# Kernel optimization log

Hardware: AMD Instinct MI355X
Metric: run time of the kernel (lower is better)

Reference implementation:

```python
import jax, jax.numpy as jnp
import numpy as np

BS, SEQ, IN_DIM, EMB = 64, 1024, 512, 1024
HID = EMB // 2  # MLP hidden = embed_dim//2 = 512
RATIO = 0.3
K = max(1, int((SEQ - 2) * RATIO))  # 306
MASK_VALUE = -10000.0
BN_EPS = 1e-5


def setup_inputs() -> dict:
    key = jax.random.key(0)
    ks = jax.random.split(key, 12)
    features = jax.random.normal(ks[0], (BS, SEQ, IN_DIM), dtype=jnp.float32)
    atten = jax.random.normal(ks[1], (BS, SEQ, SEQ), dtype=jnp.float32)
    # variable-length token ids, pad_id = 0
    lengths = jax.random.randint(ks[2], (BS,), K + 14, SEQ + 1)
    tokens = jax.random.randint(ks[3], (BS, SEQ), 1, 30000)
    text = jnp.where(jnp.arange(SEQ)[None, :] < lengths[:, None], tokens, 0).astype(jnp.int64)
    s = 0.02
    lin_w = jax.random.normal(ks[4], (IN_DIM, EMB), dtype=jnp.float32) * s
    lin_b = jnp.zeros((EMB,), dtype=jnp.float32)
    w1 = jax.random.normal(ks[5], (IN_DIM, HID), dtype=jnp.float32) * s
    b1 = jnp.zeros((HID,), dtype=jnp.float32)
    g1 = jnp.ones((HID,), dtype=jnp.float32)
    be1 = jnp.zeros((HID,), dtype=jnp.float32)
    w2 = jax.random.normal(ks[6], (HID, EMB), dtype=jnp.float32) * s
    b2 = jnp.zeros((EMB,), dtype=jnp.float32)
    return {"features": features, "atten": atten, "text": text,
            "lin_w": lin_w, "lin_b": lin_b, "w1": w1, "b1": b1,
            "g1": g1, "be1": be1, "w2": w2, "b2": b2}


def _forward(features, atten, text, lin_w, lin_b, w1, b1, g1, be1, w2, b2):
    bs, seq_len, _ = atten.shape
    atten = jnp.nan_to_num(atten, nan=0.0, posinf=0.0, neginf=0.0)
    mask = (text != 0).astype(jnp.float32)                       # (bs, seq)
    token_lens = jnp.maximum(jnp.sum(text != 0, axis=1), 1)       # (bs,)
    eos_pos = jnp.clip(token_lens - 1, 0, seq_len - 1)            # (bs,)
    # mask column 0 and column eos_pos (per batch) across all rows
    col = jnp.arange(seq_len)[None, :]
    col_mask = (col == 0) | (col == eos_pos[:, None])             # (bs, seq)
    atten = jnp.where(col_mask[:, None, :], MASK_VALUE, atten)
    # masked_fill where token is pad (columns)
    atten = jnp.where(mask[:, None, :] == 0, MASK_VALUE, atten)
    atten = jax.nn.softmax(atten, axis=1)                         # softmax over rows (dim=1)
    # select the eos row per batch, weight by mask
    atten_sel = jnp.take_along_axis(atten, eos_pos[:, None, None], axis=1)[:, 0, :] * mask
    _, topk_idx = jax.lax.top_k(atten_sel, K)                     # (bs, K)
    feats_k = jnp.take_along_axis(features, topk_idx[:, :, None], axis=1)  # (bs, K, D)
    norm = jnp.maximum(jnp.linalg.norm(feats_k, axis=-1, keepdims=True), 1e-6)
    feats_k = feats_k / norm
    cap_emb = feats_k @ lin_w + lin_b                             # (bs, K, EMB)
    # MLP: Linear -> BatchNorm1d(train-mode batch stats) -> ReLU -> Linear
    xf = feats_k.reshape(bs * K, -1)
    h = xf @ w1 + b1                                              # (bs*K, HID)
    mu = jnp.mean(h, axis=0)
    var = jnp.mean((h - mu) ** 2, axis=0)                         # biased var
    h = (h - mu) / jnp.sqrt(var + BN_EPS) * g1 + be1
    h = jax.nn.relu(h)
    feats_mlp = (h @ w2 + b2).reshape(bs, K, -1)
    fused = cap_emb + feats_mlp                                   # (bs, K, EMB)
    # variable-length top-1 pooling: max over first pool_lens[b] tokens
    pool_lens = jnp.clip(token_lens - 2, 1, K)
    valid = jnp.arange(K)[None, :] < pool_lens[:, None]           # (bs, K)
    out = jnp.max(jnp.where(valid[:, :, None], fused, -jnp.inf), axis=1)
    return out.astype(jnp.float32)


def reference(features, atten, text, lin_w, lin_b, w1, b1, g1, be1, w2, b2):
    return _forward(features, atten, text, lin_w, lin_b, w1, b1, g1, be1, w2, b2)
```

## Files before the change

### kernel.cpp

```cpp
#include <hip/hip_runtime.h>
#include <hip/hip_cooperative_groups.h>
#include <cstdint>
#include <cstddef>
#include <cmath>

namespace cg = cooperative_groups;

#define BS 64
#define SEQ 1024
#define IN_DIM 512
#define EMB 1024
#define HID 512
#define KSEL 306
#define MROWS (BS * KSEL)

typedef __bf16 bf16_t;
typedef bf16_t bf16x8 __attribute__((ext_vector_type(8)));
typedef bf16_t bf16x4 __attribute__((ext_vector_type(4)));
typedef float f32x4 __attribute__((ext_vector_type(4)));

__device__ __forceinline__ void async16(const void* g, void* l) {
  __builtin_amdgcn_global_load_lds(
      (const __attribute__((address_space(1))) unsigned int*)g,
      (__attribute__((address_space(3))) unsigned int*)l, 16, 0, 0);
}

__device__ __forceinline__ void atomicMaxF(float* a, float v) {
  if (v >= 0.f)
    atomicMax((int*)a, __float_as_int(v));
  else
    atomicMin((unsigned int*)a, __float_as_uint(v));
}

__global__ void k_meta(const int* __restrict__ text, int* __restrict__ eos,
                       float* __restrict__ out) {
  int b = blockIdx.x;
  __shared__ int cnt;
  if (threadIdx.x == 0) cnt = 0;
  __syncthreads();
  int local = 0;
  for (int i = threadIdx.x; i < SEQ; i += blockDim.x)
    local += (text[b * SEQ + i] != 0) ? 1 : 0;
  atomicAdd(&cnt, local);
  for (int c = threadIdx.x; c < EMB; c += blockDim.x)
    out[(b << 10) + c] = -INFINITY;
  __syncthreads();
  if (threadIdx.x == 0) {
    int L = cnt > 1 ? cnt : 1;
    int e = L - 1;
    if (e > SEQ - 1) e = SEQ - 1;
    eos[b] = e;
  }
}

__global__ void k_colsum(const float* __restrict__ atten, float* __restrict__ part) {
  int b = blockIdx.x;
  int r0 = blockIdx.y << 6;
  int c = threadIdx.x << 2;
  const float* base = atten + ((size_t)b << 20) + ((size_t)r0 << 10) + c;
  float4 s = {0.f, 0.f, 0.f, 0.f};
#pragma unroll 4
  for (int r = 0; r < 64; ++r) {
    float4 x = *(const float4*)(base + ((size_t)r << 10));
    s.x += __expf((isfinite(x.x) ? x.x : 0.f) - 12.f);
    s.y += __expf((isfinite(x.y) ? x.y : 0.f) - 12.f);
    s.z += __expf((isfinite(x.z) ? x.z : 0.f) - 12.f);
    s.w += __expf((isfinite(x.w) ? x.w : 0.f) - 12.f);
  }
  *(float4*)&part[((((size_t)blockIdx.y << 6) | b) << 10) | c] = s;
}

__global__ void k_topk(const float* __restrict__ atten, const int* __restrict__ text,
                       const int* __restrict__ eos, const float* __restrict__ part,
                       int* __restrict__ selidx) {
  int b = blockIdx.x;
  __shared__ float vals[SEQ];
  int e = eos[b];
  for (int c = threadIdx.x; c < SEQ; c += 256) {
    float cs = 0.f;
#pragma unroll
    for (int p = 0; p < 16; ++p) cs += part[(((p << 6) | b) << 10) | c];
    float v = atten[((size_t)b << 20) + ((size_t)e << 10) + c];
    if (!isfinite(v)) v = 0.f;
    int tok = text[(b << 10) | c];
    float res;
    if (tok == 0) res = 0.f;
    else if (c == 0 || c == e) res = 1.f / 1024.f;
    else res = __expf(v - 12.f) / cs;
    vals[c] = res;
  }
  __syncthreads();
  int i = (blockIdx.y << 8) | threadIdx.x;
  float vc = vals[i];
  int rank = 0;
  for (int j = 0; j < SEQ; ++j) {
    float vj = vals[j];
    rank += (vj > vc || (vj == vc && j < i)) ? 1 : 0;
  }
  if (rank < KSEL) selidx[b * KSEL + rank] = i;
}

__global__ void k_gather(const float* __restrict__ features, const int* __restrict__ sel,
                         bf16_t* __restrict__ xcat) {
  int row = blockIdx.x;
  int b = row / KSEL;
  int k = row - b * KSEL;
  int idx = sel[b * KSEL + k];
  const float4* src = (const float4*)(features + (((size_t)b << 10) + idx) * IN_DIM);
  float4 v = src[threadIdx.x];
  float ss = v.x * v.x + v.y * v.y + v.z * v.z + v.w * v.w;
#pragma unroll
  for (int off = 32; off > 0; off >>= 1) ss += __shfl_down(ss, off, 64);
  __shared__ float wsum[2];
  int lane = threadIdx.x & 63, wid = threadIdx.x >> 6;
  if (lane == 0) wsum[wid] = ss;
  __syncthreads();
  float total = wsum[0] + wsum[1];
  float scale = 1.f / fmaxf(sqrtf(total), 1e-6f);
  bf16x4 o;
  o[0] = (bf16_t)(v.x * scale);
  o[1] = (bf16_t)(v.y * scale);
  o[2] = (bf16_t)(v.z * scale);
  o[3] = (bf16_t)(v.w * scale);
  *(bf16x4*)(xcat + (size_t)row * EMB + (threadIdx.x << 2)) = o;
}

__global__ void k_transpose_all(const float* __restrict__ w1, const float* __restrict__ lin_w,
                                const float* __restrict__ w2, bf16_t* __restrict__ w1t,
                                bf16_t* __restrict__ wcatt) {
  __shared__ float tile[32][33];
  int by = blockIdx.y;
  const float* src; int srcld; bf16_t* dst; int dstld; int n0;
  if (by < 16)      { src = w1;    srcld = HID; dst = w1t;         dstld = IN_DIM; n0 = by << 5; }
  else if (by < 48) { src = lin_w; srcld = EMB; dst = wcatt;       dstld = EMB;    n0 = (by - 16) << 5; }
  else              { src = w2;    srcld = EMB; dst = wcatt + 512; dstld = EMB;    n0 = (by - 48) << 5; }
  int k0 = blockIdx.x << 5;
  int tx = threadIdx.x, ty = threadIdx.y;
#pragma unroll
  for (int i = 0; i < 4; i++)
    tile[ty + 8 * i][tx] = src[(size_t)(k0 + ty + 8 * i) * srcld + n0 + tx];
  __syncthreads();
#pragma unroll
  for (int i = 0; i < 4; i++)
    dst[(size_t)(n0 + ty + 8 * i) * dstld + k0 + tx] = (bf16_t)tile[tx][ty + 8 * i];
}

__global__ __launch_bounds__(512, 1) void k_gemm1_coop(
    const bf16_t* A,
    const bf16_t* __restrict__ Bt,
    const float* __restrict__ b1, const float* __restrict__ g1,
    const float* __restrict__ be1, float* stats,
    bf16_t* xcat_out) {
  __shared__ __align__(16) bf16_t As[128 * 32];
  __shared__ __align__(16) bf16_t Bs[512 * 32];
  int tid = threadIdx.x;
  int m0 = blockIdx.x << 7;
  int wave = tid >> 6, lane = tid & 63;
  int wm = (wave >> 2) << 6;
  int wn = (wave & 3) << 7;
  int lrow = lane & 15, quad = lane >> 4;

  f32x4 acc[4][8];
#pragma unroll
  for (int i = 0; i < 4; i++)
#pragma unroll
    for (int j = 0; j < 8; j++) acc[i][j] = (f32x4){0.f, 0.f, 0.f, 0.f};

  int arow = tid >> 2, ak = (tid & 3) << 3;
  const bf16_t* Ap = A + (size_t)(m0 + arow) * EMB + ak;
  int brow0 = tid >> 2, bk = (tid & 3) << 3;
  const bf16_t* Bp0 = Bt + (size_t)(brow0 + 0) * IN_DIM + bk;
  const bf16_t* Bp1 = Bt + (size_t)(brow0 + 128) * IN_DIM + bk;
  const bf16_t* Bp2 = Bt + (size_t)(brow0 + 256) * IN_DIM + bk;
  const bf16_t* Bp3 = Bt + (size_t)(brow0 + 384) * IN_DIM + bk;

  for (int k0 = 0; k0 < IN_DIM; k0 += 32) {
    async16(Ap + k0, &As[tid << 3]);
    async16(Bp0 + k0, &Bs[(tid + 0) << 3]);
    async16(Bp1 + k0, &Bs[(tid + 512) << 3]);
    async16(Bp2 + k0, &Bs[(tid + 1024) << 3]);
    async16(Bp3 + k0, &Bs[(tid + 1536) << 3]);
    __syncthreads();

    bf16x8 af[4], bfr[8];
#pragma unroll
    for (int i = 0; i < 4; i++)
      af[i] = *(const bf16x8*)&As[((wm + (i << 4) + lrow) << 5) + (quad << 3)];
#pragma unroll
    for (int j = 0; j < 8; j++)
      bfr[j] = *(const bf16x8*)&Bs[((wn + (j << 4) + lrow) << 5) + (quad << 3)];
#pragma unroll
    for (int i = 0; i < 4; i++)
#pragma unroll
      for (int j = 0; j < 8; j++)
        acc[i][j] = __builtin_amdgcn_mfma_f32_16x16x32_bf16(af[i], bfr[j], acc[i][j], 0, 0, 0);
    __syncthreads();
  }

#pragma unroll
  for (int j = 0; j < 8; j++) {
    int n = wn + (j << 4) + lrow;
    float bv = b1[n];
    float s = 0.f, qq = 0.f;
#pragma unroll
    for (int i = 0; i < 4; i++) {
#pragma unroll
      for (int rr = 0; rr < 4; rr++) {
        float v = acc[i][j][rr] + bv;
        acc[i][j][rr] = v;
        s += v;
        qq += v * v;
      }
    }
    s += __shfl_xor(s, 16, 64);
    s += __shfl_xor(s, 32, 64);
    qq += __shfl_xor(qq, 16, 64);
    qq += __shfl_xor(qq, 32, 64);
    if (quad == 0) {
      atomicAdd(&stats[n], s);
      atomicAdd(&stats[HID + n], qq);
    }
  }

  cg::this_grid().sync();

  const float inv = 1.f / (float)MROWS;
#pragma unroll
  for (int j = 0; j < 8; j++) {
    int n = wn + (j << 4) + lrow;
    float mu = stats[n] * inv;
    float var = fmaxf(stats[HID + n] * inv - mu * mu, 0.f);
    float sc = g1[n] * rsqrtf(var + 1e-5f);
    float sh = fmaf(-mu, sc, be1[n]);
#pragma unroll
    for (int i = 0; i < 4; i++) {
      int mbase = m0 + wm + (i << 4) + (quad << 2);
#pragma unroll
      for (int rr = 0; rr < 4; rr++) {
        float a = fmaxf(fmaf(acc[i][j][rr], sc, sh), 0.f);
        xcat_out[(size_t)(mbase + rr) * EMB + 512 + n] = (bf16_t)a;
      }
    }
  }
}

__global__ __launch_bounds__(256, 2) void k_gemm2(
    const bf16_t* __restrict__ A, const bf16_t* __restrict__ Bt,
    const float* __restrict__ lin_b, const float* __restrict__ b2,
    float* __restrict__ outmax) {
  __shared__ __align__(16) bf16_t As[128 * 32];
  __shared__ __align__(16) bf16_t Bs[128 * 32];
  int tid = threadIdx.x;

  int MT = gridDim.x, NT = gridDim.y;
  int nwg = MT * NT;
  int flat = blockIdx.y * MT + blockIdx.x;
  int q = nwg >> 3, r = nwg & 7;
  int xcd = flat & 7, ii = flat >> 3;
  int lin = (xcd < r ? xcd * (q + 1) : r * (q + 1) + (xcd - r) * q) + ii;
  int mtile = lin / NT;
  int ntile = lin - mtile * NT;
  int m0 = mtile << 7, n0 = ntile << 7;

  int wave = tid >> 6, lane = tid & 63;
  int wm = (wave >> 1) << 6, wn = (wave & 1) << 6;
  int lrow = lane & 15, quad = lane >> 4;

  f32x4 acc[4][4];
#pragma unroll
  for (int i = 0; i < 4; i++)
#pragma unroll
    for (int j = 0; j < 4; j++) acc[i][j] = (f32x4){0.f, 0.f, 0.f, 0.f};

  int c0 = tid, c1 = 256 + tid;
  int ar0 = c0 >> 2, ak0 = (c0 & 3) << 3;
  int ar1 = c1 >> 2, ak1 = (c1 & 3) << 3;
  const bf16_t* Ap0 = A + (size_t)(m0 + ar0) * EMB + ak0;
  const bf16_t* Ap1 = A + (size_t)(m0 + ar1) * EMB + ak1;
  const bf16_t* Bp0 = Bt + (size_t)(n0 + ar0) * EMB + ak0;
  const bf16_t* Bp1 = Bt + (size_t)(n0 + ar1) * EMB + ak1;

  for (int k0 = 0; k0 < EMB; k0 += 32) {
    async16(Ap0 + k0, &As[c0 << 3]);
    async16(Ap1 + k0, &As[c1 << 3]);
    async16(Bp0 + k0, &Bs[c0 << 3]);
    async16(Bp1 + k0, &Bs[c1 << 3]);
    __syncthreads();

    bf16x8 af[4], bfr[4];
#pragma unroll
    for (int i = 0; i < 4; i++)
      af[i] = *(const bf16x8*)&As[((wm + (i << 4) + lrow) << 5) + (quad << 3)];
#pragma unroll
    for (int j = 0; j < 4; j++)
      bfr[j] = *(const bf16x8*)&Bs[((wn + (j << 4) + lrow) << 5) + (quad << 3)];
#pragma unroll
    for (int i = 0; i < 4; i++)
#pragma unroll
      for (int j = 0; j < 4; j++)
        acc[i][j] = __builtin_amdgcn_mfma_f32_16x16x32_bf16(af[i], bfr[j], acc[i][j], 0, 0, 0);
    __syncthreads();
  }

  int mw = m0 + wm;
  int b0w = mw / KSEL;
  int cut = (b0w + 1) * KSEL;
#pragma unroll
  for (int j = 0; j < 4; j++) {
    int n = n0 + wn + (j << 4) + lrow;
    float bv = lin_b[n] + b2[n];
    float mx0 = -INFINITY, mx1 = -INFINITY;
#pragma unroll
    for (int i = 0; i < 4; i++) {
#pragma unroll
      for (int rr = 0; rr < 4; rr++) {
        int m = mw + (i << 4) + (quad << 2) + rr;
        float v = acc[i][j][rr] + bv;
        if (m < cut) mx0 = fmaxf(mx0, v);
        else mx1 = fmaxf(mx1, v);
      }
    }
    mx0 = fmaxf(mx0, __shfl_xor(mx0, 16, 64));
    mx0 = fmaxf(mx0, __shfl_xor(mx0, 32, 64));
    mx1 = fmaxf(mx1, __shfl_xor(mx1, 16, 64));
    mx1 = fmaxf(mx1, __shfl_xor(mx1, 32, 64));
    if (quad == 0) {
      atomicMaxF(&outmax[(b0w << 10) + n], mx0);
      if (cut < mw + 64) atomicMaxF(&outmax[((b0w + 1) << 10) + n], mx1);
    }
  }
}

extern "C" void kernel_launch(void* const* d_in, const int* in_sizes, int n_in,
                              void* d_out, int out_size, void* d_ws, size_t ws_size,
                              hipStream_t stream) {
  const float* features = (const float*)d_in[0];
  const float* atten    = (const float*)d_in[1];
  const int*   text     = (const int*)d_in[2];
  const float* lin_w    = (const float*)d_in[3];
  const float* lin_b    = (const float*)d_in[4];
  const float* w1       = (const float*)d_in[5];
  const float* b1       = (const float*)d_in[6];
  const float* g1       = (const float*)d_in[7];
  const float* be1      = (const float*)d_in[8];
  const float* w2       = (const float*)d_in[9];
  const float* b2       = (const float*)d_in[10];
  float* out = (float*)d_out;

  char* ws = (char*)d_ws;
  int*    eos    = (int*)(ws + 0);
  float*  stats  = (float*)(ws + 256);
  float*  part   = (float*)(ws + 8192);
  int*    selidx = (int*)(ws + 4202496UL);
  bf16_t* w1t    = (bf16_t*)(ws + 4280832UL);
  bf16_t* wcatt  = (bf16_t*)(ws + 4805120UL);
  bf16_t* xcat   = (bf16_t*)(ws + 6902272UL);

  hipMemsetAsync(stats, 0, 4096, stream);

  k_meta<<<BS, 256, 0, stream>>>(text, eos, out);
  k_colsum<<<dim3(BS, 16), 256, 0, stream>>>(atten, part);
  k_topk<<<dim3(BS, 4), 256, 0, stream>>>(atten, text, eos, part, selidx);
  k_gather<<<MROWS, 128, 0, stream>>>(features, selidx, xcat);
  k_transpose_all<<<dim3(16, 80), dim3(32, 8), 0, stream>>>(w1, lin_w, w2, w1t, wcatt);

  {
    const bf16_t* gA = xcat;
    const bf16_t* gB = w1t;
    const float* gb1 = b1;
    const float* gg1 = g1;
    const float* gbe = be1;
    float* gst = stats;
    bf16_t* gx = xcat;
    void* kargs[] = {(void*)&gA, (void*)&gB, (void*)&gb1, (void*)&gg1,
                     (void*)&gbe, (void*)&gst, (void*)&gx};
    hipLaunchCooperativeKernel((void*)k_gemm1_coop, dim3(MROWS / 128), dim3(512),
                               kargs, 0, stream);
  }

  k_gemm2<<<dim3(MROWS / 128, EMB / 128), 256, 0, stream>>>(
      xcat, wcatt, lin_b, b2, out);
}
```

Before: 622.6 us.

## Replace cooperative GEMM1 grid sync with split GEMM, BN-param and BN-apply kernels

Drops the cooperative kernel that held the whole 512-wide GEMM1 result in registers across a grid-wide barrier. GEMM1 now uses 128x128 tiles with XCD-aware tile remapping and 2 blocks per CU, and writes the pre-BN activations to a bf16 buffer while accumulating BN stats. A tiny kernel computes scale and shift, and an elementwise kernel applies BN and ReLU into the concat buffer. This aims to remove the grid sync and the low occupancy of the 512-thread, one-block-per-CU design, at the cost of an extra write and read of the hidden activations and two more launches.

After: 571.2 us. 8.3% less time.

```diff
diff --git a/kernel.cpp b/kernel.cpp
--- a/kernel.cpp
+++ b/kernel.cpp
@@ -1,10 +1,7 @@
 #include <hip/hip_runtime.h>
-#include <hip/hip_cooperative_groups.h>
 #include <cstdint>
 #include <cstddef>
 #include <cmath>
-
-namespace cg = cooperative_groups;
 
 #define BS 64
 #define SEQ 1024
@@ -145,69 +142,76 @@
     dst[(size_t)(n0 + ty + 8 * i) * dstld + k0 + tx] = (bf16_t)tile[tx][ty + 8 * i];
 }
 
-__global__ __launch_bounds__(512, 1) void k_gemm1_coop(
-    const bf16_t* A,
-    const bf16_t* __restrict__ Bt,
-    const float* __restrict__ b1, const float* __restrict__ g1,
-    const float* __restrict__ be1, float* stats,
-    bf16_t* xcat_out) {
+__global__ __launch_bounds__(256, 2) void k_gemm1(
+    const bf16_t* __restrict__ A, const bf16_t* __restrict__ Bt,
+    const float* __restrict__ b1, bf16_t* __restrict__ C,
+    float* __restrict__ stats) {
   __shared__ __align__(16) bf16_t As[128 * 32];
-  __shared__ __align__(16) bf16_t Bs[512 * 32];
+  __shared__ __align__(16) bf16_t Bs[128 * 32];
   int tid = threadIdx.x;
-  int m0 = blockIdx.x << 7;
+
+  int MT = gridDim.x, NT = gridDim.y;
+  int nwg = MT * NT;
+  int flat = blockIdx.y * MT + blockIdx.x;
+  int q = nwg >> 3, r = nwg & 7;
+  int xcd = flat & 7, ii = flat >> 3;
+  int lin = (xcd < r ? xcd * (q + 1) : r * (q + 1) + (xcd - r) * q) + ii;
+  int mtile = lin / NT;
+  int ntile = lin - mtile * NT;
+  int m0 = mtile << 7, n0 = ntile << 7;
+
   int wave = tid >> 6, lane = tid & 63;
-  int wm = (wave >> 2) << 6;
-  int wn = (wave & 3) << 7;
+  int wm = (wave >> 1) << 6, wn = (wave & 1) << 6;
   int lrow = lane & 15, quad = lane >> 4;
 
-  f32x4 acc[4][8];
+  f32x4 acc[4][4];
 #pragma unroll
   for (int i = 0; i < 4; i++)
 #pragma unroll
-    for (int j = 0; j < 8; j++) acc[i][j] = (f32x4){0.f, 0.f, 0.f, 0.f};
-
-  int arow = tid >> 2, ak = (tid & 3) << 3;
-  const bf16_t* Ap = A + (size_t)(m0 + arow) * EMB + ak;
-  int brow0 = tid >> 2, bk = (tid & 3) << 3;
-  const bf16_t* Bp0 = Bt + (size_t)(brow0 + 0) * IN_DIM + bk;
-  const bf16_t* Bp1 = Bt + (size_t)(brow0 + 128) * IN_DIM + bk;
-  const bf16_t* Bp2 = Bt + (size_t)(brow0 + 256) * IN_DIM + bk;
-  const bf16_t* Bp3 = Bt + (size_t)(brow0 + 384) * IN_DIM + bk;
+    for (int j = 0; j < 4; j++) acc[i][j] = (f32x4){0.f, 0.f, 0.f, 0.f};
+
+  int c0 = tid, c1 = 256 + tid;
+  int ar0 = c0 >> 2, ak0 = (c0 & 3) << 3;
+  int ar1 = c1 >> 2, ak1 = (c1 & 3) << 3;
+  const bf16_t* Ap0 = A + (size_t)(m0 + ar0) * EMB + ak0;
+  const bf16_t* Ap1 = A + (size_t)(m0 + ar1) * EMB + ak1;
+  const bf16_t* Bp0 = Bt + (size_t)(n0 + ar0) * IN_DIM + ak0;
+  const bf16_t* Bp1 = Bt + (size_t)(n0 + ar1) * IN_DIM + ak1;
 
   for (int k0 = 0; k0 < IN_DIM; k0 += 32) {
-    async16(Ap + k0, &As[tid << 3]);
-    async16(Bp0 + k0, &Bs[(tid + 0) << 3]);
-    async16(Bp1 + k0, &Bs[(tid + 512) << 3]);
-    async16(Bp2 + k0, &Bs[(tid + 1024) << 3]);
-    async16(Bp3 + k0, &Bs[(tid + 1536) << 3]);
+    async16(Ap0 + k0, &As[c0 << 3]);
+    async16(Ap1 + k0, &As[c1 << 3]);
+    async16(Bp0 + k0, &Bs[c0 << 3]);
+    async16(Bp1 + k0, &Bs[c1 << 3]);
     __syncthreads();
 
-    bf16x8 af[4], bfr[8];
+    bf16x8 af[4], bfr[4];
 #pragma unroll
     for (int i = 0; i < 4; i++)
       af[i] = *(const bf16x8*)&As[((wm + (i << 4) + lrow) << 5) + (quad << 3)];
 #pragma unroll
-    for (int j = 0; j < 8; j++)
+    for (int j = 0; j < 4; j++)
       bfr[j] = *(const bf16x8*)&Bs[((wn + (j << 4) + lrow) << 5) + (quad << 3)];
 #pragma unroll
     for (int i = 0; i < 4; i++)
 #pragma unroll
-      for (int j = 0; j < 8; j++)
+      for (int j = 0; j < 4; j++)
         acc[i][j] = __builtin_amdgcn_mfma_f32_16x16x32_bf16(af[i], bfr[j], acc[i][j], 0, 0, 0);
     __syncthreads();
   }
 
 #pragma unroll
-  for (int j = 0; j < 8; j++) {
-    int n = wn + (j << 4) + lrow;
+  for (int j = 0; j < 4; j++) {
+    int n = n0 + wn + (j << 4) + lrow;
     float bv = b1[n];
     float s = 0.f, qq = 0.f;
 #pragma unroll
     for (int i = 0; i < 4; i++) {
+      int mbase = m0 + wm + (i << 4) + (quad << 2);
 #pragma unroll
       for (int rr = 0; rr < 4; rr++) {
         float v = acc[i][j][rr] + bv;
-        acc[i][j][rr] = v;
+        C[(size_t)(mbase + rr) * HID + n] = (bf16_t)v;
         s += v;
         qq += v * v;
       }
@@ -221,27 +225,33 @@
       atomicAdd(&stats[HID + n], qq);
     }
   }
-
-  cg::this_grid().sync();
-
-  const float inv = 1.f / (float)MROWS;
-#pragma unroll
-  for (int j = 0; j < 8; j++) {
-    int n = wn + (j << 4) + lrow;
-    float mu = stats[n] * inv;
-    float var = fmaxf(stats[HID + n] * inv - mu * mu, 0.f);
-    float sc = g1[n] * rsqrtf(var + 1e-5f);
-    float sh = fmaf(-mu, sc, be1[n]);
-#pragma unroll
-    for (int i = 0; i < 4; i++) {
-      int mbase = m0 + wm + (i << 4) + (quad << 2);
-#pragma unroll
-      for (int rr = 0; rr < 4; rr++) {
-        float a = fmaxf(fmaf(acc[i][j][rr], sc, sh), 0.f);
-        xcat_out[(size_t)(mbase + rr) * EMB + 512 + n] = (bf16_t)a;
-      }
-    }
-  }
+}
+
+__global__ void k_bnparam(const float* __restrict__ stats, const float* __restrict__ g,
+                          const float* __restrict__ be, float* __restrict__ scsh) {
+  int c = threadIdx.x;
+  float inv = 1.f / (float)MROWS;
+  float mu = stats[c] * inv;
+  float var = fmaxf(stats[HID + c] * inv - mu * mu, 0.f);
+  float sc = g[c] * rsqrtf(var + 1e-5f);
+  scsh[c] = sc;
+  scsh[HID + c] = fmaf(-mu, sc, be[c]);
+}
+
+__global__ void k_bnapply(const bf16_t* __restrict__ h, const float* __restrict__ scsh,
+                          bf16_t* __restrict__ xcat) {
+  size_t idx = (size_t)blockIdx.x * blockDim.x + threadIdx.x;
+  bf16x8 x = ((const bf16x8*)h)[idx];
+  int c = (int)(idx & 63) << 3;
+  size_t row = idx >> 6;
+  bf16x8 o;
+#pragma unroll
+  for (int t = 0; t < 8; ++t) {
+    float v = (float)x[t];
+    float a = fmaxf(fmaf(v, scsh[c + t], scsh[HID + c + t]), 0.f);
+    o[t] = (bf16_t)a;
+  }
+  *(bf16x8*)(xcat + row * EMB + 512 + c) = o;
 }
 
 __global__ __launch_bounds__(256, 2) void k_gemm2(
@@ -350,11 +360,13 @@
   char* ws = (char*)d_ws;
   int*    eos    = (int*)(ws + 0);
   float*  stats  = (float*)(ws + 256);
-  float*  part   = (float*)(ws + 8192);
-  int*    selidx = (int*)(ws + 4202496UL);
-  bf16_t* w1t    = (bf16_t*)(ws + 4280832UL);
-  bf16_t* wcatt  = (bf16_t*)(ws + 4805120UL);
-  bf16_t* xcat   = (bf16_t*)(ws + 6902272UL);
+  float*  scsh   = (float*)(ws + 4608);
+  float*  part   = (float*)(ws + 12800);
+  int*    selidx = (int*)(ws + 4207104UL);
+  bf16_t* w1t    = (bf16_t*)(ws + 4285440UL);
+  bf16_t* wcatt  = (bf16_t*)(ws + 4809728UL);
+  bf16_t* xcat   = (bf16_t*)(ws + 6906880UL);
+  bf16_t* h      = (bf16_t*)(ws + 47014912UL);
 
   hipMemsetAsync(stats, 0, 4096, stream);
 
@@ -364,19 +376,10 @@
   k_gather<<<MROWS, 128, 0, stream>>>(features, selidx, xcat);
   k_transpose_all<<<dim3(16, 80), dim3(32, 8), 0, stream>>>(w1, lin_w, w2, w1t, wcatt);
 
-  {
-    const bf16_t* gA = xcat;
-    const bf16_t* gB = w1t;
-    const float* gb1 = b1;
-    const float* gg1 = g1;
-    const float* gbe = be1;
-    float* gst = stats;
-    bf16_t* gx = xcat;
-    void* kargs[] = {(void*)&gA, (void*)&gB, (void*)&gb1, (void*)&gg1,
-                     (void*)&gbe, (void*)&gst, (void*)&gx};
-    hipLaunchCooperativeKernel((void*)k_gemm1_coop, dim3(MROWS / 128), dim3(512),
-                               kargs, 0, stream);
-  }
+  k_gemm1<<<dim3(MROWS / 128, HID / 128), 256, 0, stream>>>(xcat, w1t, b1, h, stats);
+
+  k_bnparam<<<1, HID, 0, stream>>>(stats, g1, be1, scsh);
+  k_bnapply<<<(MROWS * (HID / 8)) / 256, 256, 0, stream>>>(h, scsh, xcat);
 
   k_gemm2<<<dim3(MROWS / 128, EMB / 128), 256, 0, stream>>>(
       xcat, wcatt, lin_b, b2, out);
```
